# Performance work log

Measured on AMD Instinct MI355X. Metric: run time of the kernel, lower is better.

## Reference

```python
import jax, jax.numpy as jnp
import numpy as np

EPS = 1e-10


def setup_inputs() -> dict:
    key = jax.random.key(0)
    k1, k2, k3, k4 = jax.random.split(key, 4)
    B = 8388608  # training interactions
    T = 8388608  # target (eval) interactions
    NUM_ITEMS = 1000000
    rating = jax.random.uniform(k1, (B,), dtype=jnp.float32)  # explicit ratings, > 0
    item = jax.random.randint(k2, (B,), 0, NUM_ITEMS, dtype=jnp.int32)
    target_item = jax.random.randint(k3, (T,), 0, NUM_ITEMS, dtype=jnp.int32)
    target_rating = jax.random.uniform(k4, (T,), dtype=jnp.float32)
    return {
        "rating": rating,
        "item": item,
        "target_item": target_item,
        "target_rating": target_rating,
        "num_items": NUM_ITEMS,
    }


def reference(rating, item, target_item, target_rating, num_items):
    # --- training accumulation (explicit mode, buffers start at zero) ---
    # torch scatters rating[j] into a dense [num_items, B] tensor at row item[j],
    # then sums over columns: this is exactly a segment-sum over item ids.
    base = jax.ops.segment_sum(rating, item, num_segments=num_items)  # [num_items]
    # count of strictly-positive ratings per item ((base > 0).sum(-1) in torch)
    count = jax.ops.segment_sum((rating > 0).astype(rating.dtype), item,
                                num_segments=num_items)  # [num_items]

    # --- lookup / prediction ---
    tb = base[target_item]   # [T]
    tc = count[target_item]  # [T]
    pred = tb / (tc + EPS)

    # fallback for unseen items: mean of per-item averages over seen items
    seen = count != 0
    safe_count = jnp.where(seen, count, 1.0)
    per_item_avg = jnp.where(seen, base / safe_count, 0.0)
    n_seen = jnp.maximum(jnp.sum(seen.astype(rating.dtype)), 1.0)
    global_mean = jnp.sum(per_item_avg) / n_seen
    pred = jnp.where(tc == 0, global_mean, pred)

    # explicit-feedback loss (MSE)
    loss = jnp.mean((pred - target_rating) ** 2)
    return pred, loss
```

## Files before the change

kernel.cpp:

```cpp
#include <hip/hip_runtime.h>

constexpr int kNumItems = 1000000;
constexpr int kXCD = 8;
constexpr int K2     = 256;
constexpr int BSH    = 12;
constexpr int BITEMS = 4096;
constexpr int P      = 512;
constexpr int CHUNK  = 16384;
constexpr int CSTG   = 48;
constexpr int CAP    = 128;
constexpr unsigned kCntShift = 26;
constexpr unsigned kFixMask  = (1u << 26) - 1u;
#define EPSF 1e-10f
#define FIX19 524288.0f
#define INV_FIX19 (1.0f / 524288.0f)

typedef int   __attribute__((ext_vector_type(4))) intv4;
typedef float __attribute__((ext_vector_type(4))) floatv4;

struct Scalars {
    double sum_avg;
    double n_seen;
    double loss;
};

__device__ __forceinline__ unsigned xcd_id() {
    return __builtin_amdgcn_s_getreg((31u << 11) | 20u) & 7u;
}

__device__ __forceinline__ double blockReduceSum(double v) {
    for (int off = 32; off > 0; off >>= 1)
        v += __shfl_down(v, off, 64);
    __shared__ double s[16];
    __syncthreads();
    const int lane = threadIdx.x & 63;
    const int wave = threadIdx.x >> 6;
    if (lane == 0) s[wave] = v;
    __syncthreads();
    const int nwaves = (blockDim.x + 63) >> 6;
    v = (threadIdx.x < nwaves) ? s[threadIdx.x] : 0.0;
    if (wave == 0) {
        for (int off = 8; off > 0; off >>= 1)
            v += __shfl_down(v, off, 64);
    }
    return v;
}

__device__ __forceinline__ unsigned pack_pair(int item, float r) {
    unsigned fix = (unsigned)(r * FIX19);
    unsigned cb  = (r > 0.0f) ? (1u << 19) : 0u;
    return ((unsigned)(item & (BITEMS - 1)) << 20) | cb | fix;
}


__global__ void scatter_kernel(const int* __restrict__ item,
                               const float* __restrict__ rating,
                               unsigned* __restrict__ cnt,
                               unsigned* __restrict__ pairs, int B) {
    __shared__ unsigned stage[K2][CSTG];
    __shared__ unsigned fill[K2];
    __shared__ unsigned flushed[K2];
    const int p = blockIdx.x;
    for (int k = threadIdx.x; k < K2; k += 256) {
        fill[k] = 0;
        flushed[k] = 0;
    }
    __syncthreads();
    const int base = p * CHUNK;
    const int f16 = threadIdx.x >> 4;
    const int lane16 = threadIdx.x & 15;
#pragma unroll 1
    for (int j = 0; j < CHUNK / 1024; ++j) {
        int e = base + j * 1024 + threadIdx.x * 4;
        if (e + 3 < B) {
            intv4   it = __builtin_nontemporal_load((const intv4*)(item + e));
            floatv4 r  = __builtin_nontemporal_load((const floatv4*)(rating + e));
            int k; unsigned s;
            k = it.x >> BSH; s = atomicAdd(&fill[k], 1u); stage[k][s % CSTG] = pack_pair(it.x, r.x);
            k = it.y >> BSH; s = atomicAdd(&fill[k], 1u); stage[k][s % CSTG] = pack_pair(it.y, r.y);
            k = it.z >> BSH; s = atomicAdd(&fill[k], 1u); stage[k][s % CSTG] = pack_pair(it.z, r.z);
            k = it.w >> BSH; s = atomicAdd(&fill[k], 1u); stage[k][s % CSTG] = pack_pair(it.w, r.w);
        } else {
            for (int q = e; q < B && q < e + 4; ++q) {
                int k = item[q] >> BSH;
                unsigned s = atomicAdd(&fill[k], 1u);
                stage[k][s % CSTG] = pack_pair(item[q], rating[q]);
            }
        }
        __syncthreads();
        for (int b = 0; b < K2 / 16; ++b) {
            int k = f16 + (b << 4);
            unsigned f = fill[k];
            unsigned g = flushed[k];
            size_t rb = ((size_t)k * P + p) * CAP;
            while ((g + 1) * 16 <= f) {
                unsigned sbase = (g * 16) % CSTG;
                unsigned v = stage[k][sbase + lane16];
                if (g * 16 < (unsigned)CAP)
                    pairs[rb + g * 16 + lane16] = v;
                ++g;
            }
            if (lane16 == 0) flushed[k] = g;
        }
        __syncthreads();
    }
    for (int b = 0; b < K2 / 16; ++b) {
        int k = f16 + (b << 4);
        unsigned f = fill[k];
        unsigned g = flushed[k];
        if (g * 16 < f && g * 16 < (unsigned)CAP) {
            size_t rb = ((size_t)k * P + p) * CAP;
            unsigned sbase = (g * 16) % CSTG;
            unsigned idx = g * 16 + lane16;
            unsigned v = (idx < f) ? stage[k][sbase + lane16] : 0u;
            pairs[rb + idx] = v;
        }
    }
    for (int k = threadIdx.x; k < K2; k += 256)
        cnt[(size_t)k * P + p] = min(fill[k], (unsigned)CAP);
}

__global__ void bucket_accum_kernel(const unsigned* __restrict__ pairs,
                                    const unsigned* __restrict__ cnt,
                                    unsigned* __restrict__ table,
                                    Scalars* sc) {
    __shared__ unsigned hist[BITEMS];
    __shared__ unsigned cnl[P];
    const int k = blockIdx.x;
    for (int i = threadIdx.x; i < BITEMS; i += 1024) hist[i] = 0;
    for (int i = threadIdx.x; i < P; i += 1024)
        cnl[i] = cnt[(size_t)k * P + i];
    __syncthreads();
    const int wave = threadIdx.x >> 6;
    const int lane = threadIdx.x & 63;
    for (int p = wave; p < P; p += 16) {
        unsigned n = cnl[p];
        size_t rb = ((size_t)k * P + p) * CAP;
        for (unsigned i = lane; i < n; i += 64) {
            unsigned v = __builtin_nontemporal_load(pairs + rb + i);
            if (v) {
                unsigned add = ((v & (1u << 19)) << 7) | (v & 0x7FFFFu);
                atomicAdd(&hist[v >> 20], add);
            }
        }
    }
    __syncthreads();
    double sum = 0.0, ns = 0.0;
    const int gbase = k * BITEMS;
    for (int i = threadIdx.x; i < BITEMS; i += 1024) {
        int g = gbase + i;
        if (g < kNumItems) {
            unsigned e = hist[i];
            table[g] = e;
            unsigned c = e >> kCntShift;
            if (c) {
                float sf = (float)(e & kFixMask) * INV_FIX19;
                sum += (double)(sf / (float)c);
                ns += 1.0;
            }
        }
    }
    sum = blockReduceSum(sum);
    ns  = blockReduceSum(ns);
    if (threadIdx.x == 0) {
        unsafeAtomicAdd(&sc->sum_avg, sum);
        unsafeAtomicAdd(&sc->n_seen, ns);
    }
}


__global__ void accum_fb_kernel(const float* __restrict__ rating,
                                const int* __restrict__ item,
                                unsigned* __restrict__ tabs,
                                int B, int lo, int hi) {
    unsigned* tab = tabs + (size_t)xcd_id() * kNumItems;
    int i4 = (blockIdx.x * blockDim.x + threadIdx.x) * 4;
    if (i4 + 3 < B) {
        intv4   it = __builtin_nontemporal_load((const intv4*)(item + i4));
        floatv4 r  = __builtin_nontemporal_load((const floatv4*)(rating + i4));
        int k[4] = {it.x, it.y, it.z, it.w};
        float rr[4] = {r.x, r.y, r.z, r.w};
#pragma unroll
        for (int q = 0; q < 4; ++q)
            if (k[q] >= lo && k[q] < hi) {
                unsigned enc = (unsigned)(rr[q] * FIX19) +
                               (rr[q] > 0.0f ? (1u << kCntShift) : 0u);
                __hip_atomic_fetch_add(tab + k[q], enc, __ATOMIC_RELAXED,
                                       __HIP_MEMORY_SCOPE_WORKGROUP);
            }
    } else {
        for (int i = i4; i < B; ++i)
            if (item[i] >= lo && item[i] < hi) {
                unsigned enc = (unsigned)(rating[i] * FIX19) +
                               (rating[i] > 0.0f ? (1u << kCntShift) : 0u);
                __hip_atomic_fetch_add(tab + item[i], enc, __ATOMIC_RELAXED,
                                       __HIP_MEMORY_SCOPE_WORKGROUP);
            }
    }
}

__global__ void merge_fb_kernel(unsigned* __restrict__ tabs, Scalars* sc, int n) {
    int i = blockIdx.x * blockDim.x + threadIdx.x;
    double sum = 0.0, ns = 0.0;
    if (i < n) {
        unsigned long long t = 0;
#pragma unroll
        for (int x = 0; x < kXCD; ++x)
            t += tabs[(size_t)x * kNumItems + i];
        unsigned e = (unsigned)t;
        tabs[i] = e;
        unsigned c = e >> kCntShift;
        if (c) {
            float sf = (float)(e & kFixMask) * INV_FIX19;
            sum = (double)(sf / (float)c);
            ns = 1.0;
        }
    }
    sum = blockReduceSum(sum);
    ns  = blockReduceSum(ns);
    if (threadIdx.x == 0) {
        unsafeAtomicAdd(&sc->sum_avg, sum);
        unsafeAtomicAdd(&sc->n_seen, ns);
    }
}


__device__ __forceinline__ float decode_pred(unsigned e, float gmf) {
    unsigned c = e >> kCntShift;
    float sf = (float)(e & kFixMask) * INV_FIX19;
    return c ? sf / ((float)c + EPSF) : gmf;
}

__device__ __forceinline__ unsigned gather_l2(const unsigned* p) {
    return __hip_atomic_load(p, __ATOMIC_RELAXED, __HIP_MEMORY_SCOPE_AGENT);
}

__global__ void pred_kernel(const unsigned* __restrict__ tab,
                            const int* __restrict__ titem,
                            const float* __restrict__ trat,
                            float* __restrict__ out,
                            double* __restrict__ loss,
                            const Scalars* __restrict__ sc,
                            int T) {
    const float gmf = (float)(sc->sum_avg / fmax(sc->n_seen, 1.0));
    const int t0 = (blockIdx.x * blockDim.x + threadIdx.x) * 16;
    double l = 0.0;
    if (t0 + 15 < T) {
        intv4 it0 = __builtin_nontemporal_load((const intv4*)(titem + t0));
        intv4 it1 = __builtin_nontemporal_load((const intv4*)(titem + t0 + 4));
        intv4 it2 = __builtin_nontemporal_load((const intv4*)(titem + t0 + 8));
        intv4 it3 = __builtin_nontemporal_load((const intv4*)(titem + t0 + 12));
        floatv4 r0 = __builtin_nontemporal_load((const floatv4*)(trat + t0));
        floatv4 r1 = __builtin_nontemporal_load((const floatv4*)(trat + t0 + 4));
        floatv4 r2 = __builtin_nontemporal_load((const floatv4*)(trat + t0 + 8));
        floatv4 r3 = __builtin_nontemporal_load((const floatv4*)(trat + t0 + 12));
        unsigned e0  = gather_l2(tab + (unsigned)it0.x);
        unsigned e1  = gather_l2(tab + (unsigned)it0.y);
        unsigned e2  = gather_l2(tab + (unsigned)it0.z);
        unsigned e3  = gather_l2(tab + (unsigned)it0.w);
        unsigned e4  = gather_l2(tab + (unsigned)it1.x);
        unsigned e5  = gather_l2(tab + (unsigned)it1.y);
        unsigned e6  = gather_l2(tab + (unsigned)it1.z);
        unsigned e7  = gather_l2(tab + (unsigned)it1.w);
        unsigned e8  = gather_l2(tab + (unsigned)it2.x);
        unsigned e9  = gather_l2(tab + (unsigned)it2.y);
        unsigned e10 = gather_l2(tab + (unsigned)it2.z);
        unsigned e11 = gather_l2(tab + (unsigned)it2.w);
        unsigned e12 = gather_l2(tab + (unsigned)it3.x);
        unsigned e13 = gather_l2(tab + (unsigned)it3.y);
        unsigned e14 = gather_l2(tab + (unsigned)it3.z);
        unsigned e15 = gather_l2(tab + (unsigned)it3.w);
        floatv4 p0, p1, p2, p3;
        p0.x = decode_pred(e0,  gmf);
        p0.y = decode_pred(e1,  gmf);
        p0.z = decode_pred(e2,  gmf);
        p0.w = decode_pred(e3,  gmf);
        p1.x = decode_pred(e4,  gmf);
        p1.y = decode_pred(e5,  gmf);
        p1.z = decode_pred(e6,  gmf);
        p1.w = decode_pred(e7,  gmf);
        p2.x = decode_pred(e8,  gmf);
        p2.y = decode_pred(e9,  gmf);
        p2.z = decode_pred(e10, gmf);
        p2.w = decode_pred(e11, gmf);
        p3.x = decode_pred(e12, gmf);
        p3.y = decode_pred(e13, gmf);
        p3.z = decode_pred(e14, gmf);
        p3.w = decode_pred(e15, gmf);
        __builtin_nontemporal_store(p0, (floatv4*)(out + t0));
        __builtin_nontemporal_store(p1, (floatv4*)(out + t0 + 4));
        __builtin_nontemporal_store(p2, (floatv4*)(out + t0 + 8));
        __builtin_nontemporal_store(p3, (floatv4*)(out + t0 + 12));
        double d;
        d = (double)p0.x - (double)r0.x; l += d * d;
        d = (double)p0.y - (double)r0.y; l += d * d;
        d = (double)p0.z - (double)r0.z; l += d * d;
        d = (double)p0.w - (double)r0.w; l += d * d;
        d = (double)p1.x - (double)r1.x; l += d * d;
        d = (double)p1.y - (double)r1.y; l += d * d;
        d = (double)p1.z - (double)r1.z; l += d * d;
        d = (double)p1.w - (double)r1.w; l += d * d;
        d = (double)p2.x - (double)r2.x; l += d * d;
        d = (double)p2.y - (double)r2.y; l += d * d;
        d = (double)p2.z - (double)r2.z; l += d * d;
        d = (double)p2.w - (double)r2.w; l += d * d;
        d = (double)p3.x - (double)r3.x; l += d * d;
        d = (double)p3.y - (double)r3.y; l += d * d;
        d = (double)p3.z - (double)r3.z; l += d * d;
        d = (double)p3.w - (double)r3.w; l += d * d;
    } else {
        for (int i = t0; i < T; ++i) {
            float p = decode_pred(tab[(unsigned)titem[i]], gmf);
            out[i] = p;
            double d = (double)p - (double)trat[i];
            l += d * d;
        }
    }
    l = blockReduceSum(l);
    if (threadIdx.x == 0) unsafeAtomicAdd(loss, l);
}

__global__ void finalize_kernel(const Scalars* __restrict__ sc,
                                float* __restrict__ out_loss, int T) {
    if (threadIdx.x == 0 && blockIdx.x == 0)
        out_loss[0] = (float)(sc->loss / (double)T);
}

extern "C" void kernel_launch(void* const* d_in, const int* in_sizes, int n_in,
                              void* d_out, int out_size, void* d_ws, size_t ws_size,
                              hipStream_t stream) {
    const float* rating = (const float*)d_in[0];
    const int*   item   = (const int*)d_in[1];
    const int*   titem  = (const int*)d_in[2];
    const float* trat   = (const float*)d_in[3];
    const int B = in_sizes[0];
    const int T = in_sizes[2];
    const int NI = kNumItems;
    const int BLK = 256;
    float* out = (float*)d_out;
    const int gPred = ((T + 15) / 16 + BLK - 1) / BLK;

    size_t u = 0;
    unsigned* pairs = (unsigned*)d_ws + 0;  u += (size_t)K2 * P * CAP;
    unsigned* cnt   = (unsigned*)d_ws + u;  u += (size_t)K2 * P;
    unsigned* table = (unsigned*)d_ws + u;  u += (size_t)NI;
    size_t sc_off = ((u * 4 + 7) / 8) * 8;
    Scalars* sc = (Scalars*)((char*)d_ws + sc_off);
    const size_t needed = sc_off + sizeof(Scalars);

    const bool fast = (ws_size >= needed) && (B <= P * CHUNK);

    if (fast) {
        (void)hipMemsetAsync(sc, 0, sizeof(Scalars), stream);
        scatter_kernel<<<P, BLK, 0, stream>>>(item, rating, cnt, pairs, B);
        bucket_accum_kernel<<<K2, 1024, 0, stream>>>(pairs, cnt, table, sc);
        pred_kernel<<<gPred, BLK, 0, stream>>>(table, titem, trat,
                                               out, &sc->loss, sc, T);
        finalize_kernel<<<1, 64, 0, stream>>>(sc, out + T, T);
    } else {
        unsigned* tabs = (unsigned*)d_ws;
        Scalars* sc2 = (Scalars*)((char*)d_ws + (size_t)kXCD * NI * sizeof(unsigned));
        (void)hipMemsetAsync(d_ws, 0,
                             (size_t)kXCD * NI * sizeof(unsigned) + sizeof(Scalars),
                             stream);
        const int gAcc = ((B + 3) / 4 + BLK - 1) / BLK;
        accum_fb_kernel<<<gAcc, BLK, 0, stream>>>(rating, item, tabs, B, 0, NI / 2);
        accum_fb_kernel<<<gAcc, BLK, 0, stream>>>(rating, item, tabs, B, NI / 2, NI);
        merge_fb_kernel<<<(NI + BLK - 1) / BLK, BLK, 0, stream>>>(tabs, sc2, NI);
        pred_kernel<<<gPred, BLK, 0, stream>>>(tabs, titem, trat,
                                               out, &sc2->loss, sc2, T);
        finalize_kernel<<<1, 64, 0, stream>>>(sc2, out + T, T);
    }
}
```

Before: 285.3 us.

## Split bucket accumulation across two blocks per bucket and add a stats merge kernel

The bucket histogram pass now launches two blocks per bucket. Each block handles half of the producer partitions and writes a partial histogram. A new table_stats kernel adds the two partials, writes the final table and reduces the seen-item statistics. Separately, the scatter kernel moves from 256-thread to 512-thread blocks, and the prediction gather switches from relaxed agent-scope atomic loads to plain loads. The aim is more parallelism in the histogram phase and cheaper gathers, at the cost of an extra kernel launch, extra partial-buffer traffic and more global double atomics.

```diff
diff --git a/kernel.cpp b/kernel.cpp
--- a/kernel.cpp
+++ b/kernel.cpp
@@ -7,6 +7,7 @@
 constexpr int BITEMS = 4096;
 constexpr int P      = 512;
 constexpr int CHUNK  = 16384;
+constexpr int SBLK   = 512;
 constexpr int CSTG   = 48;
 constexpr int CAP    = 128;
 constexpr unsigned kCntShift = 26;
@@ -24,6 +25,7 @@
     double loss;
 };
 
+
 __device__ __forceinline__ unsigned xcd_id() {
     return __builtin_amdgcn_s_getreg((31u << 11) | 20u) & 7u;
 }
@@ -51,7 +53,6 @@
     unsigned cb  = (r > 0.0f) ? (1u << 19) : 0u;
     return ((unsigned)(item & (BITEMS - 1)) << 20) | cb | fix;
 }
-
 
 __global__ void scatter_kernel(const int* __restrict__ item,
                                const float* __restrict__ rating,
@@ -61,7 +62,7 @@
     __shared__ unsigned fill[K2];
     __shared__ unsigned flushed[K2];
     const int p = blockIdx.x;
-    for (int k = threadIdx.x; k < K2; k += 256) {
+    for (int k = threadIdx.x; k < K2; k += SBLK) {
         fill[k] = 0;
         flushed[k] = 0;
     }
@@ -70,8 +71,8 @@
     const int f16 = threadIdx.x >> 4;
     const int lane16 = threadIdx.x & 15;
 #pragma unroll 1
-    for (int j = 0; j < CHUNK / 1024; ++j) {
-        int e = base + j * 1024 + threadIdx.x * 4;
+    for (int j = 0; j < CHUNK / (SBLK * 4); ++j) {
+        int e = base + j * (SBLK * 4) + threadIdx.x * 4;
         if (e + 3 < B) {
             intv4   it = __builtin_nontemporal_load((const intv4*)(item + e));
             floatv4 r  = __builtin_nontemporal_load((const floatv4*)(rating + e));
@@ -88,8 +89,8 @@
             }
         }
         __syncthreads();
-        for (int b = 0; b < K2 / 16; ++b) {
-            int k = f16 + (b << 4);
+        for (int b = 0; b < K2 / 32; ++b) {
+            int k = f16 + (b << 5);
             unsigned f = fill[k];
             unsigned g = flushed[k];
             size_t rb = ((size_t)k * P + p) * CAP;
@@ -104,8 +105,8 @@
         }
         __syncthreads();
     }
-    for (int b = 0; b < K2 / 16; ++b) {
-        int k = f16 + (b << 4);
+    for (int b = 0; b < K2 / 32; ++b) {
+        int k = f16 + (b << 5);
         unsigned f = fill[k];
         unsigned g = flushed[k];
         if (g * 16 < f && g * 16 < (unsigned)CAP) {
@@ -116,25 +117,26 @@
             pairs[rb + idx] = v;
         }
     }
-    for (int k = threadIdx.x; k < K2; k += 256)
+    for (int k = threadIdx.x; k < K2; k += SBLK)
         cnt[(size_t)k * P + p] = min(fill[k], (unsigned)CAP);
 }
 
 __global__ void bucket_accum_kernel(const unsigned* __restrict__ pairs,
                                     const unsigned* __restrict__ cnt,
-                                    unsigned* __restrict__ table,
-                                    Scalars* sc) {
+                                    unsigned* __restrict__ partial) {
     __shared__ unsigned hist[BITEMS];
-    __shared__ unsigned cnl[P];
-    const int k = blockIdx.x;
+    __shared__ unsigned cnl[P / 2];
+    const int k = blockIdx.x >> 1;
+    const int h = blockIdx.x & 1;
     for (int i = threadIdx.x; i < BITEMS; i += 1024) hist[i] = 0;
-    for (int i = threadIdx.x; i < P; i += 1024)
-        cnl[i] = cnt[(size_t)k * P + i];
+    if (threadIdx.x < P / 2)
+        cnl[threadIdx.x] = cnt[(size_t)k * P + h * (P / 2) + threadIdx.x];
     __syncthreads();
     const int wave = threadIdx.x >> 6;
     const int lane = threadIdx.x & 63;
-    for (int p = wave; p < P; p += 16) {
-        unsigned n = cnl[p];
+    for (int q = wave; q < P / 2; q += 16) {
+        int p = h * (P / 2) + q;
+        unsigned n = cnl[q];
         size_t rb = ((size_t)k * P + p) * CAP;
         for (unsigned i = lane; i < n; i += 64) {
             unsigned v = __builtin_nontemporal_load(pairs + rb + i);
@@ -145,19 +147,24 @@
         }
     }
     __syncthreads();
+    unsigned* dst = partial + ((size_t)h * K2 + k) * BITEMS;
+    for (int i = threadIdx.x; i < BITEMS; i += 1024)
+        __builtin_nontemporal_store(hist[i], dst + i);
+}
+
+__global__ void table_stats_kernel(const unsigned* __restrict__ partial,
+                                   unsigned* __restrict__ table,
+                                   Scalars* sc, int n) {
+    int i = blockIdx.x * blockDim.x + threadIdx.x;
     double sum = 0.0, ns = 0.0;
-    const int gbase = k * BITEMS;
-    for (int i = threadIdx.x; i < BITEMS; i += 1024) {
-        int g = gbase + i;
-        if (g < kNumItems) {
-            unsigned e = hist[i];
-            table[g] = e;
-            unsigned c = e >> kCntShift;
-            if (c) {
-                float sf = (float)(e & kFixMask) * INV_FIX19;
-                sum += (double)(sf / (float)c);
-                ns += 1.0;
-            }
+    if (i < n) {
+        unsigned e = partial[i] + partial[(size_t)K2 * BITEMS + i];
+        table[i] = e;
+        unsigned c = e >> kCntShift;
+        if (c) {
+            float sf = (float)(e & kFixMask) * INV_FIX19;
+            sum = (double)(sf / (float)c);
+            ns = 1.0;
         }
     }
     sum = blockReduceSum(sum);
@@ -229,10 +236,6 @@
     unsigned c = e >> kCntShift;
     float sf = (float)(e & kFixMask) * INV_FIX19;
     return c ? sf / ((float)c + EPSF) : gmf;
-}
-
-__device__ __forceinline__ unsigned gather_l2(const unsigned* p) {
-    return __hip_atomic_load(p, __ATOMIC_RELAXED, __HIP_MEMORY_SCOPE_AGENT);
 }
 
 __global__ void pred_kernel(const unsigned* __restrict__ tab,
@@ -254,22 +257,22 @@
         floatv4 r1 = __builtin_nontemporal_load((const floatv4*)(trat + t0 + 4));
         floatv4 r2 = __builtin_nontemporal_load((const floatv4*)(trat + t0 + 8));
         floatv4 r3 = __builtin_nontemporal_load((const floatv4*)(trat + t0 + 12));
-        unsigned e0  = gather_l2(tab + (unsigned)it0.x);
-        unsigned e1  = gather_l2(tab + (unsigned)it0.y);
-        unsigned e2  = gather_l2(tab + (unsigned)it0.z);
-        unsigned e3  = gather_l2(tab + (unsigned)it0.w);
-        unsigned e4  = gather_l2(tab + (unsigned)it1.x);
-        unsigned e5  = gather_l2(tab + (unsigned)it1.y);
-        unsigned e6  = gather_l2(tab + (unsigned)it1.z);
-        unsigned e7  = gather_l2(tab + (unsigned)it1.w);
-        unsigned e8  = gather_l2(tab + (unsigned)it2.x);
-        unsigned e9  = gather_l2(tab + (unsigned)it2.y);
-        unsigned e10 = gather_l2(tab + (unsigned)it2.z);
-        unsigned e11 = gather_l2(tab + (unsigned)it2.w);
-        unsigned e12 = gather_l2(tab + (unsigned)it3.x);
-        unsigned e13 = gather_l2(tab + (unsigned)it3.y);
-        unsigned e14 = gather_l2(tab + (unsigned)it3.z);
-        unsigned e15 = gather_l2(tab + (unsigned)it3.w);
+        unsigned e0  = tab[(unsigned)it0.x];
+        unsigned e1  = tab[(unsigned)it0.y];
+        unsigned e2  = tab[(unsigned)it0.z];
+        unsigned e3  = tab[(unsigned)it0.w];
+        unsigned e4  = tab[(unsigned)it1.x];
+        unsigned e5  = tab[(unsigned)it1.y];
+        unsigned e6  = tab[(unsigned)it1.z];
+        unsigned e7  = tab[(unsigned)it1.w];
+        unsigned e8  = tab[(unsigned)it2.x];
+        unsigned e9  = tab[(unsigned)it2.y];
+        unsigned e10 = tab[(unsigned)it2.z];
+        unsigned e11 = tab[(unsigned)it2.w];
+        unsigned e12 = tab[(unsigned)it3.x];
+        unsigned e13 = tab[(unsigned)it3.y];
+        unsigned e14 = tab[(unsigned)it3.z];
+        unsigned e15 = tab[(unsigned)it3.w];
         floatv4 p0, p1, p2, p3;
         p0.x = decode_pred(e0,  gmf);
         p0.y = decode_pred(e1,  gmf);
@@ -341,9 +344,10 @@
     const int gPred = ((T + 15) / 16 + BLK - 1) / BLK;
 
     size_t u = 0;
-    unsigned* pairs = (unsigned*)d_ws + 0;  u += (size_t)K2 * P * CAP;
-    unsigned* cnt   = (unsigned*)d_ws + u;  u += (size_t)K2 * P;
-    unsigned* table = (unsigned*)d_ws + u;  u += (size_t)NI;
+    unsigned* pairs   = (unsigned*)d_ws + 0;  u += (size_t)K2 * P * CAP;
+    unsigned* cnt     = (unsigned*)d_ws + u;  u += (size_t)K2 * P;
+    unsigned* partial = (unsigned*)d_ws + u;  u += (size_t)2 * K2 * BITEMS;
+    unsigned* table   = (unsigned*)d_ws + u;  u += (size_t)NI;
     size_t sc_off = ((u * 4 + 7) / 8) * 8;
     Scalars* sc = (Scalars*)((char*)d_ws + sc_off);
     const size_t needed = sc_off + sizeof(Scalars);
@@ -352,8 +356,10 @@
 
     if (fast) {
         (void)hipMemsetAsync(sc, 0, sizeof(Scalars), stream);
-        scatter_kernel<<<P, BLK, 0, stream>>>(item, rating, cnt, pairs, B);
-        bucket_accum_kernel<<<K2, 1024, 0, stream>>>(pairs, cnt, table, sc);
+        scatter_kernel<<<P, SBLK, 0, stream>>>(item, rating, cnt, pairs, B);
+        bucket_accum_kernel<<<2 * K2, 1024, 0, stream>>>(pairs, cnt, partial);
+        table_stats_kernel<<<(NI + BLK - 1) / BLK, BLK, 0, stream>>>(partial,
+                                                                     table, sc, NI);
         pred_kernel<<<gPred, BLK, 0, stream>>>(table, titem, trat,
                                                out, &sc->loss, sc, T);
         finalize_kernel<<<1, 64, 0, stream>>>(sc, out + T, T);
```

Result: slower. 340.5 us (+19.3%).
